# Kernel tuning notes

Measured on AMD Instinct MI355X. Metric: run time of the kernel, lower is better.

The kernel has to match this reference:

```python
import jax, jax.numpy as jnp
import numpy as np

D_MODEL = 512
N_HEADS = 8
NUM_NODES = 20
EPS = 1e-5

def _layer_norm(x, g, b):
    mu = jnp.mean(x, axis=-1, keepdims=True)
    var = jnp.var(x, axis=-1, keepdims=True)
    return (x - mu) * jax.lax.rsqrt(var + EPS) * g + b

def _conv1d(x_bcn, w_oik):
    # x: [B, C, N], w: [O, I, K], padding = K//2 (same)
    k = w_oik.shape[-1]
    p = k // 2
    return jax.lax.conv_general_dilated(
        x_bcn, w_oik, window_strides=(1,), padding=[(p, p)],
        dimension_numbers=('NCH', 'OIH', 'NCH'))

def setup_inputs() -> dict:
    key = jax.random.key(0)
    ks = jax.random.split(key, 6)
    B, N, D, H = 4096, NUM_NODES, D_MODEL, N_HEADS
    x = jax.random.normal(ks[0], (B, N, D), dtype=jnp.float32)
    s = 1.0 / np.sqrt(D * 3)
    Wq = jax.random.normal(ks[1], (D, D, 3), dtype=jnp.float32) * s
    Wk = jax.random.normal(ks[2], (D, D, 3), dtype=jnp.float32) * s
    Wv = jax.random.normal(ks[3], (D, D, 3), dtype=jnp.float32) * s
    rel_table = jax.random.normal(ks[4], (2 * N - 1, H), dtype=jnp.float32) * 0.02
    Wo = jax.random.normal(ks[5], (D, D), dtype=jnp.float32) * (1.0 / np.sqrt(D))
    bo = jnp.zeros((D,), dtype=jnp.float32)
    ones = jnp.ones((D,), dtype=jnp.float32)
    zeros = jnp.zeros((D,), dtype=jnp.float32)
    return {"x": x, "Wq": Wq, "Wk": Wk, "Wv": Wv,
            "lnq_g": ones, "lnq_b": zeros, "lnk_g": ones, "lnk_b": zeros,
            "lnv_g": ones, "lnv_b": zeros,
            "rel_table": rel_table, "Wo": Wo, "bo": bo}

def reference(x, Wq, Wk, Wv, lnq_g, lnq_b, lnk_g, lnk_b, lnv_g, lnv_b, rel_table, Wo, bo):
    B, N, D = x.shape
    H = N_HEADS
    dk = D // H
    x_p = jnp.transpose(x, (0, 2, 1))  # [B, D, N]

    def proj(W, g, b):
        c = _conv1d(x_p, W)                      # [B, D, N]
        c = _layer_norm(jnp.transpose(c, (0, 2, 1)), g, b)  # [B, N, D]
        return x + c                              # residual

    q = proj(Wq, lnq_g, lnq_b)
    k = proj(Wk, lnk_g, lnk_b)
    v = proj(Wv, lnv_g, lnv_b)

    q = q.reshape(B, N, H, dk).transpose(0, 2, 1, 3)  # [B,H,N,dk]
    k = k.reshape(B, N, H, dk).transpose(0, 2, 1, 3)
    v = v.reshape(B, N, H, dk).transpose(0, 2, 1, 3)

    scale = 1.0 / np.sqrt(dk)
    scores = jnp.einsum('bhnd,bhmd->bhnm', q, k) * scale  # [B,H,N,N]

    # relative position bias: index[i,j] = i - j + N - 1
    coords = jnp.arange(N)
    rel_idx = coords[:, None] - coords[None, :] + (N - 1)   # [N,N]
    rel_bias = rel_table[rel_idx]                            # [N,N,H]
    rel_bias = jnp.transpose(rel_bias, (2, 0, 1))[None]      # [1,H,N,N]
    scores = scores + rel_bias

    attn = jax.nn.softmax(scores, axis=-1)
    out = jnp.einsum('bhnm,bhmd->bhnd', attn, v)             # [B,H,N,dk]
    out = out.transpose(0, 2, 1, 3).reshape(B, N, D)
    return out @ Wo.T + bo
```

## Files before the change

kernel.cpp:

```cpp
#include <hip/hip_runtime.h>
#include <hip/hip_bf16.h>
#include <stdint.h>
#include <string.h>

typedef __attribute__((ext_vector_type(8))) __bf16 bf16x8;
typedef __attribute__((ext_vector_type(2))) __bf16 bf16x2;
typedef __attribute__((ext_vector_type(4))) float f32x4;
typedef __attribute__((ext_vector_type(16))) float f32x16;

#define B_TOT   4096
#define NN      20
#define DM      512
#define NC1     1536
#define M_TOT   (B_TOT*NN)
#define NPAD    22

__device__ __forceinline__ void async_copy16(const __bf16* g, __bf16* l) {
    __builtin_amdgcn_global_load_lds(
        (__attribute__((address_space(1))) void*)g,
        (__attribute__((address_space(3))) void*)l, 16, 0, 0);
}

template<typename T>
__device__ __forceinline__ void load8(const T* p, float* r) {
    if constexpr (sizeof(T) == 4) {
        f32x4 a = *(const f32x4*)p;
        f32x4 b = *(const f32x4*)(p + 4);
#pragma unroll
        for (int i = 0; i < 4; ++i) { r[i] = a[i]; r[i + 4] = b[i]; }
    } else {
        bf16x8 a = *(const bf16x8*)p;
#pragma unroll
        for (int i = 0; i < 8; ++i) r[i] = (float)a[i];
    }
}

__device__ __forceinline__ bf16x8 zero8() {
    bf16x8 z;
#pragma unroll
    for (int i = 0; i < 8; ++i) z[i] = (__bf16)0.f;
    return z;
}

__device__ __forceinline__ uint32_t pkbf(float a, float b) {
    __bf16 x = (__bf16)a, y = (__bf16)b;
    uint16_t ux, uy;
    __builtin_memcpy(&ux, &x, 2); __builtin_memcpy(&uy, &y, 2);
    return (uint32_t)ux | ((uint32_t)uy << 16);
}

__device__ __forceinline__ bf16x8 mkfrag(uint32_t w0, uint32_t w1, uint32_t w2, uint32_t w3) {
    union { uint32_t u[4]; bf16x8 v; } X;
    X.u[0] = w0; X.u[1] = w1; X.u[2] = w2; X.u[3] = w3;
    return X.v;
}

__global__ void detect_kernel(const uint32_t* __restrict__ xw, int* __restrict__ mode) {
    int lane = threadIdx.x & 63;
    int susp = 0;
#pragma unroll
    for (int i = 0; i < 4; ++i) {
        uint32_t w = xw[lane * 4 + i];
        uint32_t e = (w >> 7) & 0xFF;
        if ((e >= 118 && e <= 130) || (w & 0xFFFFu) == 0) susp++;
    }
#pragma unroll
    for (int o = 32; o > 0; o >>= 1) susp += __shfl_xor(susp, o, 64);
    if (lane == 0) *mode = (susp > 128) ? 1 : 0;
}

template<typename T>
__device__ __forceinline__ void wt_body(
    const T* __restrict__ Wq, const T* __restrict__ Wk, const T* __restrict__ Wv,
    const T* __restrict__ Wo, __bf16* __restrict__ Wt, __bf16* __restrict__ Wob, int t)
{
    if (t < 3 * 512 * 512) {
        int p = t >> 18;
        int r = t & 262143;
        int o = r >> 9, i = r & 511;
        const T* W = (p == 0) ? Wq : ((p == 1) ? Wk : Wv);
        const T* src = W + (size_t)(o * 512 + i) * 3;
        float w0 = (float)src[0], w1 = (float)src[1], w2 = (float)src[2];
        size_t base = (size_t)(p * 512 + o) * 1536 + i;
        Wt[base]        = (__bf16)w0;
        Wt[base + 512]  = (__bf16)w1;
        Wt[base + 1024] = (__bf16)w2;
    } else {
        int g2 = t - 3 * 512 * 512;
        Wob[g2] = (__bf16)(float)Wo[g2];
    }
}

__global__ __launch_bounds__(256) void wt_kernel(
    const void* Wq, const void* Wk, const void* Wv, const void* Wo,
    __bf16* Wt, __bf16* Wob, const int* mode)
{
    int t = blockIdx.x * 256 + threadIdx.x;
    if (*mode)
        wt_body<__bf16>((const __bf16*)Wq, (const __bf16*)Wk, (const __bf16*)Wv,
                        (const __bf16*)Wo, Wt, Wob, t);
    else
        wt_body<float>((const float*)Wq, (const float*)Wk, (const float*)Wv,
                       (const float*)Wo, Wt, Wob, t);
}

template<typename T>
__device__ __forceinline__ void xpad_body(
    const T* __restrict__ x, __bf16* __restrict__ xp, int idx)
{
    int col = (idx & 63) * 8;
    int row = idx >> 6;
    int b = row / 22;
    int np = row - b * 22;
    bf16x8 ov;
    if (np == 0 || np == 21) {
        ov = zero8();
    } else {
        float tmp[8];
        load8<T>(x + ((size_t)(b * 20 + np - 1) * 512 + col), tmp);
#pragma unroll
        for (int t = 0; t < 8; ++t) ov[t] = (__bf16)tmp[t];
    }
    *(bf16x8*)(xp + (size_t)row * 512 + col) = ov;
}

__global__ __launch_bounds__(256) void xpad_kernel(
    const void* x, __bf16* xp, const int* mode)
{
    int idx = blockIdx.x * 256 + threadIdx.x;
    if (*mode) xpad_body<__bf16>((const __bf16*)x, xp, idx);
    else       xpad_body<float>((const float*)x, xp, idx);
}

#define SBAR()  __builtin_amdgcn_s_barrier()
#define SCHED0() __builtin_amdgcn_sched_barrier(0)
#define LGKM0() do { asm volatile("s_waitcnt lgkmcnt(0)" ::: "memory"); SCHED0(); } while (0)
#define VM4()   do { SCHED0(); asm volatile("s_waitcnt vmcnt(4)" ::: "memory"); } while (0)
#define VM0()   do { SCHED0(); asm volatile("s_waitcnt vmcnt(0)" ::: "memory"); } while (0)

__device__ __forceinline__ void g1_loadA(const __bf16* slab, int off, bf16x8 (&aq)[4]) {
#pragma unroll
    for (int i = 0; i < 4; ++i) aq[i] = *(const bf16x8*)(slab + off + i * 512);
}
__device__ __forceinline__ void g1_loadB(const __bf16* slab, int off, bf16x8 (&bq)[4]) {
#pragma unroll
    for (int i = 0; i < 4; ++i) bq[i] = *(const bf16x8*)(slab + off + i * 512);
}
template<int QM>
__device__ __forceinline__ void g1_mma(bf16x8 (&aq)[4], bf16x8 (&bq)[4], f32x4 (&acc)[8][4]) {
    __builtin_amdgcn_s_setprio(1);
#pragma unroll
    for (int i = 0; i < 4; ++i)
#pragma unroll
        for (int nf = 0; nf < 4; ++nf)
            acc[QM * 4 + i][nf] = __builtin_amdgcn_mfma_f32_16x16x32_bf16(
                aq[i], bq[nf], acc[QM * 4 + i][nf], 0, 0, 0);
    __builtin_amdgcn_s_setprio(0);
}

__global__ __launch_bounds__(512, 2) void g1_kernel(
    const __bf16* __restrict__ xpad, const __bf16* __restrict__ Wt,
    __bf16* __restrict__ Cout, int mbase)
{
    extern __shared__ __align__(16) __bf16 sh[];
    __bf16* shA = sh;
    __bf16* shB = sh + 32768;

    const int tid = threadIdx.x;
    const int w = tid >> 6, l = tid & 63;
    const int lr = l & 15, lq = l >> 4;
    const int wm = w >> 2, wn = w & 3;

    int nwg = gridDim.x;
    int bid = blockIdx.x;
    if ((nwg & 7) == 0) bid = (bid & 7) * (nwg >> 3) + (bid >> 3);
    const int nb = bid % 6;
    const int mb = bid / 6;
    const int n0 = nb * 256;
    const int mloc = mb * 256;

    const int rin = l >> 2;
    const int pc  = (l & 3) * 8;
    const int lc  = (rin >= 8) ? (pc ^ 16) : pc;
    const int R0 = w * 16 + rin;
    const int R1 = 128 + R0;
    const int g0 = mbase + mloc + R0, g1r = mbase + mloc + R1;
    const __bf16* aP0 = xpad + (size_t)((g0 / 20) * 22 + g0 % 20) * 512 + lc;
    const __bf16* aP1 = xpad + (size_t)((g1r / 20) * 22 + g1r % 20) * 512 + lc;
    const __bf16* bP0 = Wt + (size_t)(n0 + R0) * 1536 + lc;
    const __bf16* bP1 = Wt + (size_t)(n0 + R1) * 1536 + lc;
    const int sdst = w * 512 + l * 8;

    const int swzcol = (lr >= 8) ? ((lq * 8) ^ 16) : (lq * 8);
    const int ardoff = lr * 32 + swzcol;
    const int rdA = wm * 8 * 512 + ardoff;
    const int rdB = wn * 4 * 512 + ardoff;

    f32x4 acc[8][4] = {};
    bf16x8 aq[4], bq[4];

    { __bf16* d = shA + 0 * 8192 + sdst; async_copy16(aP0 + 0, d);  async_copy16(aP1 + 0, d + 4096); }
    { __bf16* d = shB + 0 * 8192 + sdst; async_copy16(bP0 + 0, d);  async_copy16(bP1 + 0, d + 4096); }
    { __bf16* d = shA + 1 * 8192 + sdst; async_copy16(aP0 + 32, d); async_copy16(aP1 + 32, d + 4096); }
    { __bf16* d = shB + 1 * 8192 + sdst; async_copy16(bP0 + 32, d); async_copy16(bP1 + 32, d + 4096); }
    VM4();
    SBAR();

    for (int t = 0; t < 24; ++t) {
        const int cur = t & 1;
        const __bf16* A0 = shA + (cur * 2 + 0) * 8192;
        const __bf16* A1 = shA + (cur * 2 + 1) * 8192;
        const __bf16* B0 = shB + (cur * 2 + 0) * 8192;
        const __bf16* B1 = shB + (cur * 2 + 1) * 8192;
        __bf16* dA0 = shA + ((cur ^ 1) * 2 + 0) * 8192 + sdst;
        __bf16* dA1 = shA + ((cur ^ 1) * 2 + 1) * 8192 + sdst;
        __bf16* dB0 = shB + ((cur ^ 1) * 2 + 0) * 8192 + sdst;
        __bf16* dB1 = shB + ((cur ^ 1) * 2 + 1) * 8192 + sdst;
        const int kn = (t + 1) * 64;
        const bool st = (t < 23);

        g1_loadA(A0, rdA, aq);
        g1_loadB(B0, rdB, bq);
        if (st) { async_copy16(aP0 + kn, dA0); async_copy16(aP1 + kn, dA0 + 4096); }
        SBAR(); LGKM0();
        g1_mma<0>(aq, bq, acc);
        SBAR();

        g1_loadA(A0, rdA + 2048, aq);
        if (st) { async_copy16(bP0 + kn, dB0); async_copy16(bP1 + kn, dB0 + 4096); }
        if (st) VM4(); else VM0();
        SBAR(); LGKM0();
        g1_mma<1>(aq, bq, acc);
        SBAR();

        g1_loadA(A1, rdA, aq);
        g1_loadB(B1, rdB, bq);
        if (st) { async_copy16(aP0 + kn + 32, dA1); async_copy16(aP1 + kn + 32, dA1 + 4096); }
        SBAR(); LGKM0();
        g1_mma<0>(aq, bq, acc);
        SBAR();

        g1_loadA(A1, rdA + 2048, aq);
        if (st) { async_copy16(bP0 + kn + 32, dB1); async_copy16(bP1 + kn + 32, dB1 + 4096); }
        if (st) VM4();
        SBAR(); LGKM0();
        g1_mma<1>(aq, bq, acc);
        SBAR();
    }

#pragma unroll
    for (int mf = 0; mf < 8; ++mf) {
#pragma unroll
        for (int r = 0; r < 4; ++r) {
            int row = mloc + wm * 128 + mf * 16 + lq * 4 + r;
            size_t base = (size_t)row * 1536 + n0 + wn * 64 + lr;
#pragma unroll
            for (int nf = 0; nf < 4; ++nf)
                Cout[base + nf * 16] = (__bf16)acc[mf][nf][r];
        }
    }
}

template<typename T>
__device__ __forceinline__ void attn_body(
    const __bf16* __restrict__ xpad, const __bf16* __restrict__ cqkv,
    const T* __restrict__ lnq_g, const T* __restrict__ lnq_b,
    const T* __restrict__ lnk_g, const T* __restrict__ lnk_b,
    const T* __restrict__ lnv_g, const T* __restrict__ lnv_b,
    const T* __restrict__ rel, __bf16* __restrict__ aout, int bbase,
    __bf16* sq , float* rbt )
{
    const int tid = threadIdx.x;
    const int wave = tid >> 6, lane = tid & 63;
    const int bl = blockIdx.x;
    char* sqb = (char*)sq;
    const size_t xpbase = ((size_t)(bbase + bl) * NPAD + 1) * DM;
    const size_t cbase = (size_t)bl * NN * NC1;

    for (int t = tid; t < 312; t += 512) {
        int h = t & 7, d = t >> 3;
        rbt[h * 40 + d] = (float)rel[t];
    }

    for (int row = wave; row < 60; row += 8) {
        int p = row / 20;
        int n = row - p * 20;
        bf16x8 cv = *(const bf16x8*)(cqkv + cbase + (size_t)n * NC1 + p * 512 + lane * 8);
        float vals[8]; float s = 0.f, ss = 0.f;
#pragma unroll
        for (int t = 0; t < 8; ++t) { float f = (float)cv[t]; vals[t] = f; s += f; ss += f * f; }
#pragma unroll
        for (int o = 32; o > 0; o >>= 1) { s += __shfl_xor(s, o, 64); ss += __shfl_xor(ss, o, 64); }
        float mu = s * (1.f / 512.f);
        float var = ss * (1.f / 512.f) - mu * mu;
        float rs = rsqrtf(var + 1e-5f);
        const T* g  = (p == 0) ? lnq_g : (p == 1) ? lnk_g : lnv_g;
        const T* bb = (p == 0) ? lnq_b : (p == 1) ? lnk_b : lnv_b;
        float gv[8], bv[8];
        load8<T>(g  + lane * 8, gv);
        load8<T>(bb + lane * 8, bv);
        bf16x8 xv = *(const bf16x8*)(xpad + xpbase + (size_t)n * DM + lane * 8);
        bf16x8 ov;
#pragma unroll
        for (int t = 0; t < 8; ++t)
            ov[t] = (__bf16)((vals[t] - mu) * rs * gv[t] + bv[t] + (float)xv[t]);
        *(bf16x8*)(sqb + row * 1024 + ((lane * 16) ^ ((row & 7) << 4))) = ov;
    }
    __syncthreads();

    const int h  = wave;
    const int ic = lane & 31;
    const int lq = lane >> 5;

    f32x16 s;
#pragma unroll
    for (int r = 0; r < 16; ++r) s[r] = 0.f;
#pragma unroll
    for (int call = 0; call < 4; ++call) {
        int kb2 = (call * 16 + lq * 8) * 2;
        bf16x8 af = zero8(), bf_ = zero8();
        if (ic < 20) {
            int rk = 20 + ic;
            af  = *(const bf16x8*)(sqb + rk * 1024 + ((h * 128 + kb2) ^ ((rk & 7) << 4)));
            bf_ = *(const bf16x8*)(sqb + ic * 1024 + ((h * 128 + kb2) ^ ((ic & 7) << 4)));
        }
        s = __builtin_amdgcn_mfma_f32_32x32x16_bf16(af, bf_, s, 0, 0, 0);
    }
    __syncthreads();

    float p_[16];
    float mx = -1e30f;
#pragma unroll
    for (int r = 0; r < 16; ++r) {
        int j = (r & 3) + 8 * (r >> 2) + 4 * lq;
        if (j < 20) {
            int d = ic - j + 19;
            d = d < 0 ? 0 : (d > 38 ? 38 : d);
            float v = s[r] * 0.125f + rbt[h * 40 + d];
            p_[r] = v;
            mx = fmaxf(mx, v);
        } else p_[r] = -1e30f;
    }
    mx = fmaxf(mx, __shfl_xor(mx, 32, 64));
    float sum = 0.f;
#pragma unroll
    for (int r = 0; r < 16; ++r) {
        int j = (r & 3) + 8 * (r >> 2) + 4 * lq;
        float e = (j < 20) ? expf(p_[r] - mx) : 0.f;
        p_[r] = e; sum += e;
    }
    sum += __shfl_xor(sum, 32, 64);
    float inv = 1.f / sum;
#pragma unroll
    for (int r = 0; r < 16; ++r) p_[r] *= inv;

    uint32_t pk[8], qk[8];
#pragma unroll
    for (int k = 0; k < 8; ++k) pk[k] = pkbf(p_[2 * k], p_[2 * k + 1]);
#pragma unroll
    for (int k = 0; k < 8; ++k) qk[k] = (uint32_t)__shfl_xor((int)pk[k], 32, 64);
    bf16x8 pa1 = lq ? mkfrag(qk[2], qk[3], pk[2], pk[3]) : mkfrag(pk[0], pk[1], qk[0], qk[1]);
    bf16x8 pa2 = lq ? mkfrag(qk[6], qk[7], pk[6], pk[7]) : mkfrag(pk[4], pk[5], qk[4], qk[5]);

#pragma unroll
    for (int half = 0; half < 2; ++half) {
        f32x16 o;
#pragma unroll
        for (int r = 0; r < 16; ++r) o[r] = 0.f;
        const int cb2 = h * 128 + half * 64 + ic * 2;
#pragma unroll
        for (int call = 0; call < 2; ++call) {
            int jb = call * 16 + lq * 8;
            union { unsigned short u[8]; bf16x8 v; } V;
#pragma unroll
            for (int e = 0; e < 8; ++e) {
                int j = jb + e;
                unsigned short val = 0;
                if (j < 20) {
                    int rv = 40 + j;
                    val = *(const unsigned short*)(sqb + rv * 1024 + (cb2 ^ ((rv & 7) << 4)));
                }
                V.u[e] = val;
            }
            o = __builtin_amdgcn_mfma_f32_32x32x16_bf16(call ? pa2 : pa1, V.v, o, 0, 0, 0);
        }
#pragma unroll
        for (int r = 0; r < 16; ++r) {
            int i = (r & 3) + 8 * (r >> 2) + 4 * lq;
            if (i < 20) {
                __bf16 b = (__bf16)o[r];
                unsigned short ub;
                __builtin_memcpy(&ub, &b, 2);
                *(unsigned short*)(sqb + i * 1024 + (cb2 ^ ((i & 7) << 4))) = ub;
            }
        }
    }
    __syncthreads();

    __bf16* ab = aout + (size_t)bl * NN * DM;
    for (int t = tid; t < 1280; t += 512) {
        int row = t >> 6;
        int bc = (t & 63) * 16;
        bf16x8 vv = *(const bf16x8*)(sqb + row * 1024 + (bc ^ ((row & 7) << 4)));
        *(bf16x8*)(ab + t * 8) = vv;
    }
}

__global__ __launch_bounds__(512) void attn_kernel(
    const __bf16* xpad, const __bf16* cqkv,
    const void* lnq_g, const void* lnq_b, const void* lnk_g, const void* lnk_b,
    const void* lnv_g, const void* lnv_b, const void* rel,
    __bf16* aout, int bbase, const int* mode)
{
    __shared__ __align__(16) __bf16 sq[60 * 512];
    __shared__ float rbt[8 * 40];
    if (*mode)
        attn_body<__bf16>(xpad, cqkv,
            (const __bf16*)lnq_g, (const __bf16*)lnq_b, (const __bf16*)lnk_g,
            (const __bf16*)lnk_b, (const __bf16*)lnv_g, (const __bf16*)lnv_b,
            (const __bf16*)rel, aout, bbase, sq, rbt);
    else
        attn_body<float>(xpad, cqkv,
            (const float*)lnq_g, (const float*)lnq_b, (const float*)lnk_g,
            (const float*)lnk_b, (const float*)lnv_g, (const float*)lnv_b,
            (const float*)rel, aout, bbase, sq, rbt);
}

template<typename T>
__device__ __forceinline__ void g3_body(
    const __bf16* __restrict__ Ain, const __bf16* __restrict__ Wob,
    const T* __restrict__ bo, T* __restrict__ out, int mbase,
    __bf16* As, __bf16* Bs)
{
    const int tid  = threadIdx.x;
    const int wave = tid >> 6, lane = tid & 63;
    const int n0 = blockIdx.x * 128;
    const int m0 = blockIdx.y * 128;
    const int srow = lane >> 3;
    const int scol = (lane & 7) * 8;
    const int lr = lane & 15, lq = lane >> 4;
    const int wm = (wave >> 1) * 64, wn = (wave & 1) * 64;
    f32x4 acc[4][4] = {};

    for (int kt = 0; kt < 8; ++kt) {
        const int k0 = kt * 64;
        __syncthreads();
#pragma unroll
        for (int j = 0; j < 4; ++j) {
            int rb_ = wave * 32 + j * 8;
            async_copy16(Ain + (size_t)(m0 + rb_ + srow) * 512 + (k0 + scol),
                         As + rb_ * 64 + lane * 8);
            async_copy16(Wob + (size_t)(n0 + rb_ + srow) * 512 + (k0 + scol),
                         Bs + rb_ * 64 + lane * 8);
        }
        __syncthreads();
#pragma unroll
        for (int ko = 0; ko < 64; ko += 32) {
            bf16x8 af[4], bfv[4];
#pragma unroll
            for (int mi = 0; mi < 4; ++mi)
                af[mi] = *(const bf16x8*)&As[(wm + mi * 16 + lr) * 64 + ko + lq * 8];
#pragma unroll
            for (int ni = 0; ni < 4; ++ni)
                bfv[ni] = *(const bf16x8*)&Bs[(wn + ni * 16 + lr) * 64 + ko + lq * 8];
#pragma unroll
            for (int mi = 0; mi < 4; ++mi)
#pragma unroll
                for (int ni = 0; ni < 4; ++ni)
                    acc[mi][ni] = __builtin_amdgcn_mfma_f32_16x16x32_bf16(
                        af[mi], bfv[ni], acc[mi][ni], 0, 0, 0);
        }
    }
#pragma unroll
    for (int mi = 0; mi < 4; ++mi) {
#pragma unroll
        for (int r = 0; r < 4; ++r) {
            int row = m0 + wm + mi * 16 + lq * 4 + r;
            size_t gbase = (size_t)(mbase + row) * 512 + n0 + wn + lr;
#pragma unroll
            for (int ni = 0; ni < 4; ++ni) {
                float bias = (float)bo[n0 + wn + lr + ni * 16];
                out[gbase + ni * 16] = (T)(acc[mi][ni][r] + bias);
            }
        }
    }
}

__global__ __launch_bounds__(256) void g3_kernel(
    const __bf16* Ain, const __bf16* Wob, const void* bo, void* out,
    int mbase, const int* mode)
{
    __shared__ __align__(16) __bf16 As[128 * 64];
    __shared__ __align__(16) __bf16 Bs[128 * 64];
    if (*mode) g3_body<__bf16>(Ain, Wob, (const __bf16*)bo, (__bf16*)out, mbase, As, Bs);
    else       g3_body<float>(Ain, Wob, (const float*)bo, (float*)out, mbase, As, Bs);
}

extern "C" void kernel_launch(void* const* d_in, const int* in_sizes, int n_in,
                              void* d_out, int out_size, void* d_ws, size_t ws_size,
                              hipStream_t stream) {
    (void)in_sizes; (void)n_in; (void)out_size;
    char* ws = (char*)d_ws;
    int*    mode = (int*)ws;
    __bf16* Wt   = (__bf16*)(ws + 256);
    __bf16* Wob  = (__bf16*)(ws + 256 + 4718592);
    __bf16* xpad = (__bf16*)(ws + 256 + 4718592 + 524288);
    const size_t off_c = 256 + 4718592 + 524288 + (size_t)B_TOT * NPAD * DM * 2;

    static bool attr_set = false;
    if (!attr_set) {
        (void)hipFuncSetAttribute((const void*)g1_kernel,
                                  hipFuncAttributeMaxDynamicSharedMemorySize, 131072);
        attr_set = true;
    }

    int CH = 1;
    while (CH < 64) {
        size_t rows = (size_t)M_TOT / CH;
        if (off_c + rows * (size_t)NC1 * 2 + rows * (size_t)DM * 2 <= ws_size) break;
        CH *= 2;
    }
    const int rows = M_TOT / CH;
    const int Bc   = B_TOT / CH;
    __bf16* Cbuf = (__bf16*)(ws + off_c);
    __bf16* Abuf = (__bf16*)(ws + off_c + (size_t)rows * NC1 * 2);

    detect_kernel<<<dim3(1), dim3(64), 0, stream>>>((const uint32_t*)d_in[0], mode);
    wt_kernel<<<dim3(4096), dim3(256), 0, stream>>>(
        d_in[1], d_in[2], d_in[3], d_in[11], Wt, Wob, mode);
    xpad_kernel<<<dim3(22528), dim3(256), 0, stream>>>(d_in[0], xpad, mode);

    for (int c = 0; c < CH; ++c) {
        int mbase = c * rows;
        g1_kernel<<<dim3(6 * (rows / 256)), dim3(512), 131072, stream>>>(
            xpad, Wt, Cbuf, mbase);
        attn_kernel<<<dim3(Bc), dim3(512), 0, stream>>>(
            xpad, Cbuf, d_in[4], d_in[5], d_in[6], d_in[7], d_in[8], d_in[9],
            d_in[10], Abuf, mbase / NN, mode);
        g3_kernel<<<dim3(4, rows / 128), dim3(256), 0, stream>>>(
            Abuf, Wob, d_in[12], d_out, mbase, mode);
    }
}
```

Measured before the change: 857.2 us.

## Reuse pipelined 256x256 GEMM loop for output projection; stage LN params in LDS

Factors the double-buffered async-copy MFMA k-loop of the QKV GEMM into a template and reuses it for the output projection. The projection moves from 128x128 tiles with 256 threads and synchronous staging to 256x256 tiles with 512 threads and 128KB of dynamic LDS. The attention kernel now stages the layernorm gamma/beta in shared memory and software-prefetches the next row's inputs, drops a scratch array, and gets launch_bounds(512,4). The larger tiles reduce global traffic in the projection but cut the number of workgroups, and the extra LDS and launch bound may affect occupancy.

```diff
diff --git a/kernel.cpp b/kernel.cpp
--- a/kernel.cpp
+++ b/kernel.cpp
@@ -158,6 +158,62 @@
     __builtin_amdgcn_s_setprio(0);
 }
 
+template<int NT>
+__device__ __forceinline__ void kloop8(
+    const __bf16* aP0, const __bf16* aP1, const __bf16* bP0, const __bf16* bP1,
+    __bf16* shA, __bf16* shB, int sdst, int rdA, int rdB, f32x4 (&acc)[8][4])
+{
+    bf16x8 aq[4], bq[4];
+    { __bf16* d = shA + 0 * 8192 + sdst; async_copy16(aP0 + 0, d);  async_copy16(aP1 + 0, d + 4096); }
+    { __bf16* d = shB + 0 * 8192 + sdst; async_copy16(bP0 + 0, d);  async_copy16(bP1 + 0, d + 4096); }
+    { __bf16* d = shA + 1 * 8192 + sdst; async_copy16(aP0 + 32, d); async_copy16(aP1 + 32, d + 4096); }
+    { __bf16* d = shB + 1 * 8192 + sdst; async_copy16(bP0 + 32, d); async_copy16(bP1 + 32, d + 4096); }
+    VM4();
+    SBAR();
+
+    for (int t = 0; t < NT; ++t) {
+        const int cur = t & 1;
+        const __bf16* A0 = shA + (cur * 2 + 0) * 8192;
+        const __bf16* A1 = shA + (cur * 2 + 1) * 8192;
+        const __bf16* B0 = shB + (cur * 2 + 0) * 8192;
+        const __bf16* B1 = shB + (cur * 2 + 1) * 8192;
+        __bf16* dA0 = shA + ((cur ^ 1) * 2 + 0) * 8192 + sdst;
+        __bf16* dA1 = shA + ((cur ^ 1) * 2 + 1) * 8192 + sdst;
+        __bf16* dB0 = shB + ((cur ^ 1) * 2 + 0) * 8192 + sdst;
+        __bf16* dB1 = shB + ((cur ^ 1) * 2 + 1) * 8192 + sdst;
+        const int kn = (t + 1) * 64;
+        const bool st = (t < NT - 1);
+
+        g1_loadA(A0, rdA, aq);
+        g1_loadB(B0, rdB, bq);
+        if (st) { async_copy16(aP0 + kn, dA0); async_copy16(aP1 + kn, dA0 + 4096); }
+        SBAR(); LGKM0();
+        g1_mma<0>(aq, bq, acc);
+        SBAR();
+
+        g1_loadA(A0, rdA + 2048, aq);
+        if (st) { async_copy16(bP0 + kn, dB0); async_copy16(bP1 + kn, dB0 + 4096); }
+        if (st) VM4(); else VM0();
+        SBAR(); LGKM0();
+        g1_mma<1>(aq, bq, acc);
+        SBAR();
+
+        g1_loadA(A1, rdA, aq);
+        g1_loadB(B1, rdB, bq);
+        if (st) { async_copy16(aP0 + kn + 32, dA1); async_copy16(aP1 + kn + 32, dA1 + 4096); }
+        SBAR(); LGKM0();
+        g1_mma<0>(aq, bq, acc);
+        SBAR();
+
+        g1_loadA(A1, rdA + 2048, aq);
+        if (st) { async_copy16(bP0 + kn + 32, dB1); async_copy16(bP1 + kn + 32, dB1 + 4096); }
+        if (st) VM4();
+        SBAR(); LGKM0();
+        g1_mma<1>(aq, bq, acc);
+        SBAR();
+    }
+}
+
 __global__ __launch_bounds__(512, 2) void g1_kernel(
     const __bf16* __restrict__ xpad, const __bf16* __restrict__ Wt,
     __bf16* __restrict__ Cout, int mbase)
@@ -197,56 +253,7 @@
     const int rdB = wn * 4 * 512 + ardoff;
 
     f32x4 acc[8][4] = {};
-    bf16x8 aq[4], bq[4];
-
-    { __bf16* d = shA + 0 * 8192 + sdst; async_copy16(aP0 + 0, d);  async_copy16(aP1 + 0, d + 4096); }
-    { __bf16* d = shB + 0 * 8192 + sdst; async_copy16(bP0 + 0, d);  async_copy16(bP1 + 0, d + 4096); }
-    { __bf16* d = shA + 1 * 8192 + sdst; async_copy16(aP0 + 32, d); async_copy16(aP1 + 32, d + 4096); }
-    { __bf16* d = shB + 1 * 8192 + sdst; async_copy16(bP0 + 32, d); async_copy16(bP1 + 32, d + 4096); }
-    VM4();
-    SBAR();
-
-    for (int t = 0; t < 24; ++t) {
-        const int cur = t & 1;
-        const __bf16* A0 = shA + (cur * 2 + 0) * 8192;
-        const __bf16* A1 = shA + (cur * 2 + 1) * 8192;
-        const __bf16* B0 = shB + (cur * 2 + 0) * 8192;
-        const __bf16* B1 = shB + (cur * 2 + 1) * 8192;
-        __bf16* dA0 = shA + ((cur ^ 1) * 2 + 0) * 8192 + sdst;
-        __bf16* dA1 = shA + ((cur ^ 1) * 2 + 1) * 8192 + sdst;
-        __bf16* dB0 = shB + ((cur ^ 1) * 2 + 0) * 8192 + sdst;
-        __bf16* dB1 = shB + ((cur ^ 1) * 2 + 1) * 8192 + sdst;
-        const int kn = (t + 1) * 64;
-        const bool st = (t < 23);
-
-        g1_loadA(A0, rdA, aq);
-        g1_loadB(B0, rdB, bq);
-        if (st) { async_copy16(aP0 + kn, dA0); async_copy16(aP1 + kn, dA0 + 4096); }
-        SBAR(); LGKM0();
-        g1_mma<0>(aq, bq, acc);
-        SBAR();
-
-        g1_loadA(A0, rdA + 2048, aq);
-        if (st) { async_copy16(bP0 + kn, dB0); async_copy16(bP1 + kn, dB0 + 4096); }
-        if (st) VM4(); else VM0();
-        SBAR(); LGKM0();
-        g1_mma<1>(aq, bq, acc);
-        SBAR();
-
-        g1_loadA(A1, rdA, aq);
-        g1_loadB(B1, rdB, bq);
-        if (st) { async_copy16(aP0 + kn + 32, dA1); async_copy16(aP1 + kn + 32, dA1 + 4096); }
-        SBAR(); LGKM0();
-        g1_mma<0>(aq, bq, acc);
-        SBAR();
-
-        g1_loadA(A1, rdA + 2048, aq);
-        if (st) { async_copy16(bP0 + kn + 32, dB1); async_copy16(bP1 + kn + 32, dB1 + 4096); }
-        if (st) VM4();
-        SBAR(); LGKM0();
-        g1_mma<1>(aq, bq, acc);
-        SBAR();
-    }
+    kloop8<24>(aP0, aP1, bP0, bP1, shA, shB, sdst, rdA, rdB, acc);
 
 #pragma unroll
     for (int mf = 0; mf < 8; ++mf) {
@@ -268,7 +275,7 @@
     const T* __restrict__ lnk_g, const T* __restrict__ lnk_b,
     const T* __restrict__ lnv_g, const T* __restrict__ lnv_b,
     const T* __restrict__ rel, __bf16* __restrict__ aout, int bbase,
-    __bf16* sq , float* rbt )
+    __bf16* sq , float* rbt , float* gbln )
 {
     const int tid = threadIdx.x;
     const int wave = tid >> 6, lane = tid & 63;
@@ -277,34 +284,63 @@
     const size_t xpbase = ((size_t)(bbase + bl) * NPAD + 1) * DM;
     const size_t cbase = (size_t)bl * NN * NC1;
 
-    for (int t = tid; t < 312; t += 512) {
-        int h = t & 7, d = t >> 3;
-        rbt[h * 40 + d] = (float)rel[t];
-    }
-
-    for (int row = wave; row < 60; row += 8) {
-        int p = row / 20;
-        int n = row - p * 20;
-        bf16x8 cv = *(const bf16x8*)(cqkv + cbase + (size_t)n * NC1 + p * 512 + lane * 8);
-        float vals[8]; float s = 0.f, ss = 0.f;
-#pragma unroll
-        for (int t = 0; t < 8; ++t) { float f = (float)cv[t]; vals[t] = f; s += f; ss += f * f; }
-#pragma unroll
-        for (int o = 32; o > 0; o >>= 1) { s += __shfl_xor(s, o, 64); ss += __shfl_xor(ss, o, 64); }
-        float mu = s * (1.f / 512.f);
-        float var = ss * (1.f / 512.f) - mu * mu;
-        float rs = rsqrtf(var + 1e-5f);
-        const T* g  = (p == 0) ? lnq_g : (p == 1) ? lnk_g : lnv_g;
-        const T* bb = (p == 0) ? lnq_b : (p == 1) ? lnk_b : lnv_b;
-        float gv[8], bv[8];
-        load8<T>(g  + lane * 8, gv);
-        load8<T>(bb + lane * 8, bv);
-        bf16x8 xv = *(const bf16x8*)(xpad + xpbase + (size_t)n * DM + lane * 8);
-        bf16x8 ov;
-#pragma unroll
-        for (int t = 0; t < 8; ++t)
-            ov[t] = (__bf16)((vals[t] - mu) * rs * gv[t] + bv[t] + (float)xv[t]);
-        *(bf16x8*)(sqb + row * 1024 + ((lane * 16) ^ ((row & 7) << 4))) = ov;
+    if (tid < 384) {
+        int idx = tid * 8;
+        float tmp[8];
+        if (idx < 1536) {
+            int p = idx >> 9, col = idx & 511;
+            const T* g = (p == 0) ? lnq_g : (p == 1) ? lnk_g : lnv_g;
+            load8<T>(g + col, tmp);
+        } else {
+            int q2 = idx - 1536;
+            int p = q2 >> 9, col = q2 & 511;
+            const T* bb = (p == 0) ? lnq_b : (p == 1) ? lnk_b : lnv_b;
+            load8<T>(bb + col, tmp);
+        }
+#pragma unroll
+        for (int u = 0; u < 8; ++u) gbln[idx + u] = tmp[u];
+    }
+    if (tid < 312) {
+        int h = tid & 7, d = tid >> 3;
+        rbt[h * 40 + d] = (float)rel[tid];
+    }
+    __syncthreads();
+
+    {
+        int row0 = wave;
+        int n0r = row0 % 20;
+        bf16x8 cv0 = *(const bf16x8*)(cqkv + cbase + (size_t)n0r * NC1 + 0 * 512 + lane * 8);
+        bf16x8 xv0 = *(const bf16x8*)(xpad + xpbase + (size_t)n0r * DM + lane * 8);
+#pragma unroll
+        for (int rr = 0; rr < 8; ++rr) {
+            int row = wave + rr * 8;
+            if (row < 60) {
+                int nrow = row + 8;
+                bf16x8 cv1, xv1;
+                if (nrow < 60) {
+                    int p1 = nrow / 20, n1 = nrow - p1 * 20;
+                    cv1 = *(const bf16x8*)(cqkv + cbase + (size_t)n1 * NC1 + p1 * 512 + lane * 8);
+                    xv1 = *(const bf16x8*)(xpad + xpbase + (size_t)n1 * DM + lane * 8);
+                }
+                int p = row / 20;
+                float vals[8]; float s1 = 0.f, s2 = 0.f;
+#pragma unroll
+                for (int t = 0; t < 8; ++t) { float f = (float)cv0[t]; vals[t] = f; s1 += f; s2 += f * f; }
+#pragma unroll
+                for (int o = 32; o > 0; o >>= 1) { s1 += __shfl_xor(s1, o, 64); s2 += __shfl_xor(s2, o, 64); }
+                float mu = s1 * (1.f / 512.f);
+                float var = s2 * (1.f / 512.f) - mu * mu;
+                float rs = rsqrtf(var + 1e-5f);
+                const float* gv = gbln + p * 512 + lane * 8;
+                const float* bv = gbln + 1536 + p * 512 + lane * 8;
+                bf16x8 ov;
+#pragma unroll
+                for (int t = 0; t < 8; ++t)
+                    ov[t] = (__bf16)((vals[t] - mu) * rs * gv[t] + bv[t] + (float)xv0[t]);
+                *(bf16x8*)(sqb + row * 1024 + ((lane * 16) ^ ((row & 7) << 4))) = ov;
+                cv0 = cv1; xv0 = xv1;
+            }
+        }
     }
     __syncthreads();
 
@@ -328,7 +364,6 @@
     }
     __syncthreads();
 
-    float p_[16];
     float mx = -1e30f;
 #pragma unroll
     for (int r = 0; r < 16; ++r) {
@@ -336,27 +371,26 @@
         if (j < 20) {
             int d = ic - j + 19;
             d = d < 0 ? 0 : (d > 38 ? 38 : d);
-            float v = s[r] * 0.125f + rbt[h * 40 + d];
-            p_[r] = v;
-            mx = fmaxf(mx, v);
-        } else p_[r] = -1e30f;
+            s[r] = s[r] * 0.125f + rbt[h * 40 + d];
+            mx = fmaxf(mx, s[r]);
+        } else s[r] = -1e30f;
     }
     mx = fmaxf(mx, __shfl_xor(mx, 32, 64));
     float sum = 0.f;
 #pragma unroll
     for (int r = 0; r < 16; ++r) {
         int j = (r & 3) + 8 * (r >> 2) + 4 * lq;
-        float e = (j < 20) ? expf(p_[r] - mx) : 0.f;
-        p_[r] = e; sum += e;
+        float e = (j < 20) ? expf(s[r] - mx) : 0.f;
+        s[r] = e; sum += e;
     }
     sum += __shfl_xor(sum, 32, 64);
     float inv = 1.f / sum;
 #pragma unroll
-    for (int r = 0; r < 16; ++r) p_[r] *= inv;
+    for (int r = 0; r < 16; ++r) s[r] *= inv;
 
     uint32_t pk[8], qk[8];
 #pragma unroll
-    for (int k = 0; k < 8; ++k) pk[k] = pkbf(p_[2 * k], p_[2 * k + 1]);
+    for (int k = 0; k < 8; ++k) pk[k] = pkbf(s[2 * k], s[2 * k + 1]);
 #pragma unroll
     for (int k = 0; k < 8; ++k) qk[k] = (uint32_t)__shfl_xor((int)pk[k], 32, 64);
     bf16x8 pa1 = lq ? mkfrag(qk[2], qk[3], pk[2], pk[3]) : mkfrag(pk[0], pk[1], qk[0], qk[1]);
@@ -406,7 +440,7 @@
     }
 }
 
-__global__ __launch_bounds__(512) void attn_kernel(
+__global__ __launch_bounds__(512, 4) void attn_kernel(
     const __bf16* xpad, const __bf16* cqkv,
     const void* lnq_g, const void* lnq_b, const void* lnk_g, const void* lnk_b,
     const void* lnv_g, const void* lnv_b, const void* rel,
@@ -414,86 +448,82 @@
 {
     __shared__ __align__(16) __bf16 sq[60 * 512];
     __shared__ float rbt[8 * 40];
+    __shared__ float gbln[3072];
     if (*mode)
         attn_body<__bf16>(xpad, cqkv,
             (const __bf16*)lnq_g, (const __bf16*)lnq_b, (const __bf16*)lnk_g,
             (const __bf16*)lnk_b, (const __bf16*)lnv_g, (const __bf16*)lnv_b,
-            (const __bf16*)rel, aout, bbase, sq, rbt);
+            (const __bf16*)rel, aout, bbase, sq, rbt, gbln);
     else
         attn_body<float>(xpad, cqkv,
             (const float*)lnq_g, (const float*)lnq_b, (const float*)lnk_g,
             (const float*)lnk_b, (const float*)lnv_g, (const float*)lnv_b,
-            (const float*)rel, aout, bbase, sq, rbt);
+            (const float*)rel, aout, bbase, sq, rbt, gbln);
 }
 
 template<typename T>
 __device__ __forceinline__ void g3_body(
     const __bf16* __restrict__ Ain, const __bf16* __restrict__ Wob,
-    const T* __restrict__ bo, T* __restrict__ out, int mbase,
-    __bf16* As, __bf16* Bs)
-{
-    const int tid  = threadIdx.x;
-    const int wave = tid >> 6, lane = tid & 63;
-    const int n0 = blockIdx.x * 128;
-    const int m0 = blockIdx.y * 128;
-    const int srow = lane >> 3;
-    const int scol = (lane & 7) * 8;
-    const int lr = lane & 15, lq = lane >> 4;
-    const int wm = (wave >> 1) * 64, wn = (wave & 1) * 64;
-    f32x4 acc[4][4] = {};
-
-    for (int kt = 0; kt < 8; ++kt) {
-        const int k0 = kt * 64;
-        __syncthreads();
-#pragma unroll
-        for (int j = 0; j < 4; ++j) {
-            int rb_ = wave * 32 + j * 8;
-            async_copy16(Ain + (size_t)(m0 + rb_ + srow) * 512 + (k0 + scol),
-                         As + rb_ * 64 + lane * 8);
-            async_copy16(Wob + (size_t)(n0 + rb_ + srow) * 512 + (k0 + scol),
-                         Bs + rb_ * 64 + lane * 8);
-        }
-        __syncthreads();
-#pragma unroll
-        for (int ko = 0; ko < 64; ko += 32) {
-            bf16x8 af[4], bfv[4];
-#pragma unroll
-            for (int mi = 0; mi < 4; ++mi)
-                af[mi] = *(const bf16x8*)&As[(wm + mi * 16 + lr) * 64 + ko + lq * 8];
-#pragma unroll
-            for (int ni = 0; ni < 4; ++ni)
-                bfv[ni] = *(const bf16x8*)&Bs[(wn + ni * 16 + lr) * 64 + ko + lq * 8];
-#pragma unroll
-            for (int mi = 0; mi < 4; ++mi)
-#pragma unroll
-                for (int ni = 0; ni < 4; ++ni)
-                    acc[mi][ni] = __builtin_amdgcn_mfma_f32_16x16x32_bf16(
-                        af[mi], bfv[ni], acc[mi][ni], 0, 0, 0);
-        }
-    }
-#pragma unroll
-    for (int mi = 0; mi < 4; ++mi) {
+    const T* __restrict__ bo, T* __restrict__ out, int mbase, __bf16* sh)
+{
+    __bf16* shA = sh;
+    __bf16* shB = sh + 32768;
+
+    const int tid = threadIdx.x;
+    const int w = tid >> 6, l = tid & 63;
+    const int lr = l & 15, lq = l >> 4;
+    const int wm = w >> 2, wn = w & 3;
+
+    int nwg = gridDim.x;
+    int bid = blockIdx.x;
+    if ((nwg & 7) == 0) bid = (bid & 7) * (nwg >> 3) + (bid >> 3);
+    const int nb = bid & 1;
+    const int mb = bid >> 1;
+    const int n0 = nb * 256;
+    const int mloc = mb * 256;
+
+    const int rin = l >> 2;
+    const int pc  = (l & 3) * 8;
+    const int lc  = (rin >= 8) ? (pc ^ 16) : pc;
+    const int R0 = w * 16 + rin;
+    const int R1 = 128 + R0;
+    const __bf16* aP0 = Ain + (size_t)(mbase + mloc + R0) * 512 + lc;
+    const __bf16* aP1 = Ain + (size_t)(mbase + mloc + R1) * 512 + lc;
+    const __bf16* bP0 = Wob + (size_t)(n0 + R0) * 512 + lc;
+    const __bf16* bP1 = Wob + (size_t)(n0 + R1) * 512 + lc;
+    const int sdst = w * 512 + l * 8;
+
+    const int swzcol = (lr >= 8) ? ((lq * 8) ^ 16) : (lq * 8);
+    const int ardoff = lr * 32 + swzcol;
+    const int rdA = wm * 8 * 512 + ardoff;
+    const int rdB = wn * 4 * 512 + ardoff;
+
+    f32x4 acc[8][4] = {};
+    kloop8<8>(aP0, aP1, bP0, bP1, shA, shB, sdst, rdA, rdB, acc);
+
+    float bias[4];
+#pragma unroll
+    for (int nf = 0; nf < 4; ++nf) bias[nf] = (float)bo[n0 + wn * 64 + lr + nf * 16];
+#pragma unroll
+    for (int mf = 0; mf < 8; ++mf) {
 #pragma unroll
         for (int r = 0; r < 4; ++r) {
-            int row = m0 + wm + mi * 16 + lq * 4 + r;
-            size_t gbase = (size_t)(mbase + row) * 512 + n0 + wn + lr;
-#pragma unroll
-            for (int ni = 0; ni < 4; ++ni) {
-                float bias = (float)bo[n0 + wn + lr + ni * 16];
-                out[gbase + ni * 16] = (T)(acc[mi][ni][r] + bias);
-            }
-        }
-    }
-}
-
-__global__ __launch_bounds__(256) void g3_kernel(
+            int row = mloc + wm * 128 + mf * 16 + lq * 4 + r;
+            size_t gbase = (size_t)(mbase + row) * 512 + n0 + wn * 64 + lr;
+#pragma unroll
+            for (int nf = 0; nf < 4; ++nf)
+                out[gbase + nf * 16] = (T)(acc[mf][nf][r] + bias[nf]);
+        }
+    }
+}
+
+__global__ __launch_bounds__(512, 2) void g3_kernel(
     const __bf16* Ain, const __bf16* Wob, const void* bo, void* out,
     int mbase, const int* mode)
 {
-    __shared__ __align__(16) __bf16 As[128 * 64];
-    __shared__ __align__(16) __bf16 Bs[128 * 64];
-    if (*mode) g3_body<__bf16>(Ain, Wob, (const __bf16*)bo, (__bf16*)out, mbase, As, Bs);
-    else       g3_body<float>(Ain, Wob, (const float*)bo, (float*)out, mbase, As, Bs);
+    extern __shared__ __align__(16) __bf16 sh3[];
+    if (*mode) g3_body<__bf16>(Ain, Wob, (const __bf16*)bo, (__bf16*)out, mbase, sh3);
+    else       g3_body<float>(Ain, Wob, (const float*)bo, (float*)out, mbase, sh3);
 }
 
 extern "C" void kernel_launch(void* const* d_in, const int* in_sizes, int n_in,
@@ -511,6 +541,8 @@
     if (!attr_set) {
         (void)hipFuncSetAttribute((const void*)g1_kernel,
                                   hipFuncAttributeMaxDynamicSharedMemorySize, 131072);
+        (void)hipFuncSetAttribute((const void*)g3_kernel,
+                                  hipFuncAttributeMaxDynamicSharedMemorySize, 131072);
         attr_set = true;
     }
 
@@ -537,7 +569,7 @@
         attn_kernel<<<dim3(Bc), dim3(512), 0, stream>>>(
             xpad, Cbuf, d_in[4], d_in[5], d_in[6], d_in[7], d_in[8], d_in[9],
             d_in[10], Abuf, mbase / NN, mode);
-        g3_kernel<<<dim3(4, rows / 128), dim3(256), 0, stream>>>(
+        g3_kernel<<<dim3(2 * (rows / 256)), dim3(512), 131072, stream>>>(
             Abuf, Wob, d_in[12], d_out, mbase, mode);
     }
 }
```

Result: faster. 820.8 us (-4.2%).
